# Optimization experiments

Hardware: AMD Instinct MI355X
Metric: run time of the kernel (lower is better)

Reference implementation:

```python
import jax, jax.numpy as jnp
import numpy as np

N_NODES = 100000
N_EDGES = 3200000
IN_F = 128
HEADS = 8
OUT_C = 2  # GATConv out_channels hardcoded to 2 in the source
NEG_SLOPE = 0.2  # PyG GATConv default leaky_relu slope


def setup_inputs() -> dict:
    key = jax.random.key(0)
    ks = jax.random.split(key, 9)
    x = jax.random.normal(ks[0], (N_NODES, IN_F), dtype=jnp.float32)
    edge_index = jax.random.randint(ks[1], (2, N_EDGES), 0, N_NODES, dtype=jnp.int64)
    edge_attr = jax.random.uniform(ks[2], (N_EDGES, 1), dtype=jnp.float32)
    s = 1.0 / np.sqrt(IN_F)
    W = jax.random.normal(ks[3], (IN_F, HEADS * OUT_C), dtype=jnp.float32) * s
    att_src = jax.random.normal(ks[4], (HEADS, OUT_C), dtype=jnp.float32) * 0.5
    att_dst = jax.random.normal(ks[5], (HEADS, OUT_C), dtype=jnp.float32) * 0.5
    bias_gat = jnp.zeros((HEADS * OUT_C,), dtype=jnp.float32)
    W_fc = jax.random.normal(ks[6], (HEADS * OUT_C, 2), dtype=jnp.float32) * 0.25
    b_fc = jnp.zeros((2,), dtype=jnp.float32)
    return {"x": x, "edge_index": edge_index, "edge_attr": edge_attr,
            "W": W, "att_src": att_src, "att_dst": att_dst,
            "bias_gat": bias_gat, "W_fc": W_fc, "b_fc": b_fc}


def reference(x, edge_index, edge_attr, W, att_src, att_dst, bias_gat, W_fc, b_fc):
    # edge_attr is ignored: GATConv was built without edge_dim, matching the source.
    N = x.shape[0]
    # PyG GATConv adds self-loops by default
    loops = jnp.arange(N, dtype=edge_index.dtype)
    src = jnp.concatenate([edge_index[0], loops])  # [E']
    dst = jnp.concatenate([edge_index[1], loops])  # [E']

    h = (x @ W).reshape(N, HEADS, OUT_C)                 # [N,H,C]
    a_src = jnp.einsum('nhc,hc->nh', h, att_src)          # [N,H]
    a_dst = jnp.einsum('nhc,hc->nh', h, att_dst)          # [N,H]

    logits = jax.nn.leaky_relu(a_src[src] + a_dst[dst], negative_slope=NEG_SLOPE)  # [E',H]
    # segment softmax over edges grouped by destination node (self-loops ensure non-empty segments)
    seg_max = jax.ops.segment_max(logits, dst, num_segments=N)   # [N,H]
    p = jnp.exp(logits - seg_max[dst])                            # [E',H]
    seg_sum = jax.ops.segment_sum(p, dst, num_segments=N)         # [N,H]
    alpha = p / seg_sum[dst]                                      # [E',H]

    msg = alpha[:, :, None] * h[src]                              # [E',H,C]
    agg = jax.ops.segment_sum(msg, dst, num_segments=N)           # [N,H,C]
    gat_out = agg.reshape(N, HEADS * OUT_C) + bias_gat            # concat heads + bias
    return gat_out @ W_fc + b_fc                                  # [N,2]
```

## Files before the change

### kernel.cpp

```cpp
#include <hip/hip_runtime.h>
#include <hip/hip_fp16.h>

#define N_NODES 100000
#define IN_F 128
#define NF 16
#define HEADS 8
#define NEG_SLOPE 0.2f
#define LOG2E 1.44269504f

#define RB 256
#define LOG_RB 8
#define NB 391
#define SBITS 17
#define SMASK ((1u << SBITS) - 1)
#define BIN_C 4096
#define CAPB 9024
#define HCAP 4736


__device__ __forceinline__ void phase1_body(
    int pb, const float* __restrict__ x, const float* __restrict__ W,
    __half* __restrict__ rec, float* Ws)
{
    int t = threadIdx.x;
    for (int i = t; i < IN_F * NF; i += 512) Ws[i] = W[i];
    __syncthreads();

    int tid  = pb * 512 + t;
    int node = tid >> 4;
    int j    = tid & 15;
    if (node >= N_NODES) return;

    const float4* xr4 = (const float4*)(x + (size_t)node * IN_F);
    float acc = 0.f;
    #pragma unroll 8
    for (int k4 = 0; k4 < IN_F / 4; ++k4) {
        float4 xv = xr4[k4];
        acc = fmaf(xv.x, Ws[(4 * k4 + 0) * NF + j], acc);
        acc = fmaf(xv.y, Ws[(4 * k4 + 1) * NF + j], acc);
        acc = fmaf(xv.z, Ws[(4 * k4 + 2) * NF + j], acc);
        acc = fmaf(xv.w, Ws[(4 * k4 + 3) * NF + j], acc);
    }
    rec[(size_t)node * NF + j] = __float2half(acc);
}

__global__ __launch_bounds__(512) void fused_p1_bin(
    const int* __restrict__ ei, int* __restrict__ bin_cursor,
    unsigned* __restrict__ bins,
    const float* __restrict__ x, const float* __restrict__ W,
    __half* __restrict__ rec, int E, int SB)
{
    __shared__ union {
        struct {
            unsigned staging[BIN_C];
            unsigned short bin16[BIN_C];
            int hist[NB], offs[NB], cur[NB], gbase[NB];
            int wsum[8], woff[8];
        } b;
        float Ws[IN_F * NF];
    } sm;

    int idx = blockIdx.x;
    bool is_bin = (idx % 5 == 0) && (idx / 5 < SB);
    if (!is_bin) {
        int cb = (idx + 4) / 5; if (cb > SB) cb = SB;
        phase1_body(idx - cb, x, W, rec, sm.Ws);
        return;
    }

    int t = threadIdx.x;
    int base = (idx / 5) * BIN_C;
    int n_valid = E - base;
    if (n_valid > BIN_C) n_valid = BIN_C;
    if (n_valid < 0) n_valid = 0;

    int es[8], ed[8];
    #pragma unroll
    for (int k = 0; k < 8; ++k) {
        int i = t + 512 * k;
        bool v = i < n_valid;
        es[k] = v ? ei[base + i] : 0;
        ed[k] = v ? ei[E + base + i] : -1;
    }

    if (t < NB) sm.b.hist[t] = 0;
    __syncthreads();

    #pragma unroll
    for (int k = 0; k < 8; ++k)
        if (ed[k] >= 0) atomicAdd(&sm.b.hist[ed[k] >> LOG_RB], 1);
    __syncthreads();

    int sum = (t < NB) ? sm.b.hist[t] : 0;
    int lane = t & 63, wid = t >> 6;
    int v = sum;
    #pragma unroll
    for (int o = 1; o < 64; o <<= 1) {
        int u = __shfl_up(v, o);
        if (lane >= o) v += u;
    }
    if (lane == 63) sm.b.wsum[wid] = v;
    __syncthreads();
    if (t == 0) { int r = 0; for (int w = 0; w < 8; ++w) { sm.b.woff[w] = r; r += sm.b.wsum[w]; } }
    __syncthreads();
    int run = sm.b.woff[wid] + v - sum;
    if (t < NB) { sm.b.offs[t] = run; sm.b.cur[t] = run; }
    __syncthreads();
    if (t < NB)
        sm.b.gbase[t] = sm.b.hist[t] ? atomicAdd(&bin_cursor[t], sm.b.hist[t]) : 0;
    __syncthreads();

    #pragma unroll
    for (int k = 0; k < 8; ++k) {
        if (ed[k] >= 0) {
            int b = ed[k] >> LOG_RB;
            int slot = atomicAdd(&sm.b.cur[b], 1);
            sm.b.staging[slot] = ((unsigned)(ed[k] & (RB - 1)) << SBITS) | (unsigned)es[k];
            sm.b.bin16[slot] = (unsigned short)b;
        }
    }
    __syncthreads();

    for (int i = t; i < n_valid; i += 512) {
        int b = sm.b.bin16[i];
        int pos = sm.b.gbase[b] + (i - sm.b.offs[b]);
        if (pos < CAPB) bins[(size_t)b * CAPB + pos] = sm.b.staging[i];
    }
}

__global__ __launch_bounds__(512) void accum5_kernel(
    const unsigned* __restrict__ bins, const int* __restrict__ bin_cursor,
    const __half* __restrict__ rec,
    const float* __restrict__ att_src, const float* __restrict__ att_dst,
    const float* __restrict__ bias, const float* __restrict__ Wfc,
    const float* __restrict__ bfc, float* __restrict__ out)
{
    __shared__ unsigned staging[HCAP];
    __shared__ int hist[128], offs[129], cur[128];

    int t = threadIdx.x;
    int sb   = blockIdx.x >> 1;
    int half = blockIdx.x & 1;
    int node0 = sb * RB + half * 128;

    if (t < 128) hist[t] = 0;
    __syncthreads();

    int cnt = bin_cursor[sb];
    if (cnt > CAPB) cnt = CAPB;
    const unsigned* seg = bins + (size_t)sb * CAPB;

    unsigned rcache[18];
    int nk = 0;
    for (int i = t; i < cnt; i += 512) rcache[nk++] = seg[i];

    for (int k = 0; k < nk; ++k) {
        int dl = rcache[k] >> SBITS;
        if ((dl >> 7) == half) atomicAdd(&hist[dl & 127], 1);
    }
    __syncthreads();

    if (t < 64) {
        int h0 = hist[2 * t], h1 = hist[2 * t + 1];
        int v = h0 + h1;
        int inc = v;
        #pragma unroll
        for (int o = 1; o < 64; o <<= 1) {
            int u = __shfl_up(inc, o);
            if (t >= o) inc += u;
        }
        int ex = inc - v;
        offs[2 * t] = ex;          cur[2 * t] = ex;
        offs[2 * t + 1] = ex + h0; cur[2 * t + 1] = ex + h0;
        if (t == 63) offs[128] = inc;
    }
    __syncthreads();

    for (int k = 0; k < nk; ++k) {
        unsigned r = rcache[k];
        int dl = r >> SBITS;
        if ((dl >> 7) == half) {
            int slot = atomicAdd(&cur[dl & 127], 1);
            if (slot < HCAP) staging[slot] = r & SMASK;
        }
    }
    __syncthreads();

    int wv = t >> 6, lane = t & 63;
    int h_id = lane & 7, e_off = lane >> 3;

    float as0 = att_src[2 * h_id] * LOG2E, as1 = att_src[2 * h_id + 1] * LOG2E;
    float ad0 = att_dst[2 * h_id] * LOG2E, ad1 = att_dst[2 * h_id + 1] * LOG2E;
    float b0 = bias[2 * h_id], b1 = bias[2 * h_id + 1];
    float w00 = Wfc[(2 * h_id) * 2 + 0],     w01 = Wfc[(2 * h_id) * 2 + 1];
    float w10 = Wfc[(2 * h_id + 1) * 2 + 0], w11 = Wfc[(2 * h_id + 1) * 2 + 1];
    float c0 = bfc[0], c1 = bfc[1];

    for (int k = 0; k < 16; ++k) {
        int ln = wv + 8 * k;
        int n = node0 + ln;
        if (n >= N_NODES) break;
        int st  = offs[ln];
        int end = offs[ln + 1];
        if (st > HCAP) st = HCAP;
        if (end > HCAP) end = HCAP;
        int deg = end - st;

        __half2 hn = *(const __half2*)(rec + (size_t)n * NF + 2 * h_id);
        float hn0 = __half2float(hn.x), hn1 = __half2float(hn.y);
        float adst_h = ad0 * hn0 + ad1 * hn1;

        float den = 0.f, num0 = 0.f, num1 = 0.f;

        for (int i = e_off; i < deg; i += 8) {
            int s = staging[st + i];
            __half2 hs = *(const __half2*)(rec + (size_t)s * NF + 2 * h_id);
            float h0 = __half2float(hs.x), h1 = __half2float(hs.y);
            float l = fmaf(as0, h0, fmaf(as1, h1, adst_h));
            l = l > 0.f ? l : NEG_SLOPE * l;
            float p = exp2f(l);
            den += p;
            num0 = fmaf(p, h0, num0);
            num1 = fmaf(p, h1, num1);
        }
        #pragma unroll
        for (int m = 8; m < 64; m <<= 1) {
            den  += __shfl_xor(den,  m);
            num0 += __shfl_xor(num0, m);
            num1 += __shfl_xor(num1, m);
        }
        {
            float l = fmaf(as0, hn0, fmaf(as1, hn1, adst_h));
            l = l > 0.f ? l : NEG_SLOPE * l;
            float p = exp2f(l);
            den += p;
            num0 = fmaf(p, hn0, num0);
            num1 = fmaf(p, hn1, num1);
        }
        float g0 = num0 / den + b0;
        float g1 = num1 / den + b1;
        float o0 = g0 * w00 + g1 * w10;
        float o1 = g0 * w01 + g1 * w11;
        #pragma unroll
        for (int m = 1; m < 8; m <<= 1) {
            o0 += __shfl_xor(o0, m);
            o1 += __shfl_xor(o1, m);
        }
        if (lane == 0) {
            float2 res = { o0 + c0, o1 + c1 };
            *(float2*)(out + (size_t)n * 2) = res;
        }
    }
}

extern "C" void kernel_launch(void* const* d_in, const int* in_sizes, int n_in,
                              void* d_out, int out_size, void* d_ws, size_t ws_size,
                              hipStream_t stream)
{
    const float* x       = (const float*)d_in[0];
    const int*   ei      = (const int*)d_in[1];
    const float* W       = (const float*)d_in[3];
    const float* att_src = (const float*)d_in[4];
    const float* att_dst = (const float*)d_in[5];
    const float* bias    = (const float*)d_in[6];
    const float* Wfc     = (const float*)d_in[7];
    const float* bfc     = (const float*)d_in[8];
    float*       out     = (float*)d_out;

    const int E  = in_sizes[1] / 2;
    const int SB = (E + BIN_C - 1) / BIN_C;
    const int PB = (N_NODES * 16 + 511) / 512;

    __half* rec        = (__half*)d_ws;
    int*    bin_cursor = (int*)((char*)d_ws + (size_t)N_NODES * NF * 2);
    size_t  bins_off   = (((size_t)((char*)bin_cursor - (char*)d_ws)) + NB * 4 + 4095) & ~(size_t)4095;
    unsigned* bins     = (unsigned*)((char*)d_ws + bins_off);

    hipMemsetAsync(bin_cursor, 0, NB * sizeof(int), stream);

    fused_p1_bin<<<SB + PB, 512, 0, stream>>>(
        ei, bin_cursor, bins, x, W, rec, E, SB);
    accum5_kernel<<<2 * NB, 512, 0, stream>>>(
        bins, bin_cursor, rec, att_src, att_dst, bias, Wfc, bfc, out);
}
```

Baseline: 217.9 us.

## Process each destination bin in one 1024-thread block and split matmul accumulators

The accumulation kernel now has one 1024-thread block handle a full 256-node bin, where before two 512-thread blocks each read the whole bin and kept only their half. This halves global reads of the bin records and removes the half-filter branches. In exchange it uses larger LDS staging (CAPB entries) and fewer, bigger blocks, which may lower occupancy. The projection loop also uses two independent accumulators to shorten the FMA dependency chain.

```diff
diff --git a/kernel.cpp b/kernel.cpp
--- a/kernel.cpp
+++ b/kernel.cpp
@@ -15,7 +15,6 @@
 #define SMASK ((1u << SBITS) - 1)
 #define BIN_C 4096
 #define CAPB 9024
-#define HCAP 4736
 
 
 __device__ __forceinline__ void phase1_body(
@@ -32,16 +31,21 @@
     if (node >= N_NODES) return;
 
     const float4* xr4 = (const float4*)(x + (size_t)node * IN_F);
-    float acc = 0.f;
+    float acc0 = 0.f, acc1 = 0.f;
     #pragma unroll 8
-    for (int k4 = 0; k4 < IN_F / 4; ++k4) {
-        float4 xv = xr4[k4];
-        acc = fmaf(xv.x, Ws[(4 * k4 + 0) * NF + j], acc);
-        acc = fmaf(xv.y, Ws[(4 * k4 + 1) * NF + j], acc);
-        acc = fmaf(xv.z, Ws[(4 * k4 + 2) * NF + j], acc);
-        acc = fmaf(xv.w, Ws[(4 * k4 + 3) * NF + j], acc);
-    }
-    rec[(size_t)node * NF + j] = __float2half(acc);
+    for (int k4 = 0; k4 < IN_F / 4; k4 += 2) {
+        float4 xa = xr4[k4];
+        float4 xb = xr4[k4 + 1];
+        acc0 = fmaf(xa.x, Ws[(4 * k4 + 0) * NF + j], acc0);
+        acc0 = fmaf(xa.y, Ws[(4 * k4 + 1) * NF + j], acc0);
+        acc0 = fmaf(xa.z, Ws[(4 * k4 + 2) * NF + j], acc0);
+        acc0 = fmaf(xa.w, Ws[(4 * k4 + 3) * NF + j], acc0);
+        acc1 = fmaf(xb.x, Ws[(4 * k4 + 4) * NF + j], acc1);
+        acc1 = fmaf(xb.y, Ws[(4 * k4 + 5) * NF + j], acc1);
+        acc1 = fmaf(xb.z, Ws[(4 * k4 + 6) * NF + j], acc1);
+        acc1 = fmaf(xb.w, Ws[(4 * k4 + 7) * NF + j], acc1);
+    }
+    rec[(size_t)node * NF + j] = __float2half(acc0 + acc1);
 }
 
 __global__ __launch_bounds__(512) void fused_p1_bin(
@@ -128,41 +132,39 @@
     }
 }
 
-__global__ __launch_bounds__(512) void accum5_kernel(
+__global__ __launch_bounds__(1024) void accum6_kernel(
     const unsigned* __restrict__ bins, const int* __restrict__ bin_cursor,
     const __half* __restrict__ rec,
     const float* __restrict__ att_src, const float* __restrict__ att_dst,
     const float* __restrict__ bias, const float* __restrict__ Wfc,
     const float* __restrict__ bfc, float* __restrict__ out)
 {
-    __shared__ unsigned staging[HCAP];
-    __shared__ int hist[128], offs[129], cur[128];
+    __shared__ unsigned staging[CAPB];
+    __shared__ int hist[RB], offs[RB + 1], cur[RB];
 
     int t = threadIdx.x;
-    int sb   = blockIdx.x >> 1;
-    int half = blockIdx.x & 1;
-    int node0 = sb * RB + half * 128;
-
-    if (t < 128) hist[t] = 0;
-    __syncthreads();
-
-    int cnt = bin_cursor[sb];
+    int b = blockIdx.x;
+    int node0 = b * RB;
+
+    if (t < RB) hist[t] = 0;
+    __syncthreads();
+
+    int cnt = bin_cursor[b];
     if (cnt > CAPB) cnt = CAPB;
-    const unsigned* seg = bins + (size_t)sb * CAPB;
-
-    unsigned rcache[18];
+    const unsigned* seg = bins + (size_t)b * CAPB;
+
+    unsigned rcache[9];
     int nk = 0;
-    for (int i = t; i < cnt; i += 512) rcache[nk++] = seg[i];
-
-    for (int k = 0; k < nk; ++k) {
-        int dl = rcache[k] >> SBITS;
-        if ((dl >> 7) == half) atomicAdd(&hist[dl & 127], 1);
-    }
+    for (int i = t; i < cnt; i += 1024) rcache[nk++] = seg[i];
+
+    for (int k = 0; k < nk; ++k)
+        atomicAdd(&hist[rcache[k] >> SBITS], 1);
     __syncthreads();
 
     if (t < 64) {
-        int h0 = hist[2 * t], h1 = hist[2 * t + 1];
-        int v = h0 + h1;
+        int h0 = hist[4 * t], h1 = hist[4 * t + 1];
+        int h2 = hist[4 * t + 2], h3 = hist[4 * t + 3];
+        int v = h0 + h1 + h2 + h3;
         int inc = v;
         #pragma unroll
         for (int o = 1; o < 64; o <<= 1) {
@@ -170,19 +172,18 @@
             if (t >= o) inc += u;
         }
         int ex = inc - v;
-        offs[2 * t] = ex;          cur[2 * t] = ex;
-        offs[2 * t + 1] = ex + h0; cur[2 * t + 1] = ex + h0;
-        if (t == 63) offs[128] = inc;
+        offs[4 * t] = ex;     cur[4 * t] = ex;     ex += h0;
+        offs[4 * t + 1] = ex; cur[4 * t + 1] = ex; ex += h1;
+        offs[4 * t + 2] = ex; cur[4 * t + 2] = ex; ex += h2;
+        offs[4 * t + 3] = ex; cur[4 * t + 3] = ex;
+        if (t == 63) offs[RB] = inc;
     }
     __syncthreads();
 
     for (int k = 0; k < nk; ++k) {
         unsigned r = rcache[k];
-        int dl = r >> SBITS;
-        if ((dl >> 7) == half) {
-            int slot = atomicAdd(&cur[dl & 127], 1);
-            if (slot < HCAP) staging[slot] = r & SMASK;
-        }
+        int slot = atomicAdd(&cur[r >> SBITS], 1);
+        staging[slot] = r & SMASK;
     }
     __syncthreads();
 
@@ -196,15 +197,12 @@
     float w10 = Wfc[(2 * h_id + 1) * 2 + 0], w11 = Wfc[(2 * h_id + 1) * 2 + 1];
     float c0 = bfc[0], c1 = bfc[1];
 
-    for (int k = 0; k < 16; ++k) {
-        int ln = wv + 8 * k;
+    for (int k = 0; k < RB / 16; ++k) {
+        int ln = wv + 16 * k;
         int n = node0 + ln;
         if (n >= N_NODES) break;
         int st  = offs[ln];
-        int end = offs[ln + 1];
-        if (st > HCAP) st = HCAP;
-        if (end > HCAP) end = HCAP;
-        int deg = end - st;
+        int deg = offs[ln + 1] - st;
 
         __half2 hn = *(const __half2*)(rec + (size_t)n * NF + 2 * h_id);
         float hn0 = __half2float(hn.x), hn1 = __half2float(hn.y);
@@ -280,6 +278,6 @@
 
     fused_p1_bin<<<SB + PB, 512, 0, stream>>>(
         ei, bin_cursor, bins, x, W, rec, E, SB);
-    accum5_kernel<<<2 * NB, 512, 0, stream>>>(
+    accum6_kernel<<<NB, 1024, 0, stream>>>(
         bins, bin_cursor, rec, att_src, att_dst, bias, Wfc, bfc, out);
 }
```

After: 210.7 us. -3.3%, faster.
